# Performance work log

Measured on AMD Instinct MI355X. Metric: run time of the kernel, lower is better.

The kernel has to match this reference:

```python
import jax, jax.numpy as jnp
import numpy as np

B, N, F_IN, F_OUT = 8, 2048, 256, 64
ALPHA = 0.2          # LeakyReLU negative slope
NEG_INF = -9e15      # matches -9000000000000000.0 in the torch code


def setup_inputs() -> dict:
    key = jax.random.key(0)
    k = jax.random.split(key, 7)
    x = jax.random.normal(k[0], (B, N, F_IN), dtype=jnp.float32)
    adj = jax.random.randint(k[1], (B, N, N), 0, 2, dtype=jnp.int32)
    # W: nn.Linear(in_features, out_features)
    W = jax.random.normal(k[2], (F_IN, F_OUT), dtype=jnp.float32) / np.sqrt(F_IN)
    b_W = jax.random.normal(k[3], (F_OUT,), dtype=jnp.float32) * 0.01
    # a: nn.Linear(2*out_features, 1); decomposed as a_src (first F_OUT rows,
    # multiplies h_i) and a_dst (last F_OUT rows, multiplies h_j) + bias.
    a_src = jax.random.normal(k[4], (F_OUT,), dtype=jnp.float32) / np.sqrt(2 * F_OUT)
    a_dst = jax.random.normal(k[5], (F_OUT,), dtype=jnp.float32) / np.sqrt(2 * F_OUT)
    a_b = jax.random.normal(k[6], (), dtype=jnp.float32) * 0.01
    return {"x": x, "adj": adj, "W": W, "b_W": b_W,
            "a_src": a_src, "a_dst": a_dst, "a_b": a_b}


def reference(x, adj, W, b_W, a_src, a_dst, a_b):
    # h = W(input): [B, N, F_OUT]
    h = jnp.einsum('bnf,fo->bno', x, W) + b_W
    # Additive attention decomposition: a([h_i || h_j]) = a_src.h_i + a_dst.h_j + b
    # (avoids materializing the [B, N, N, 2F] concat tensor of the original)
    src = jnp.einsum('bno,o->bn', h, a_src)  # row term  (h_i)
    dst = jnp.einsum('bno,o->bn', h, a_dst)  # col term  (h_j)
    e = jax.nn.leaky_relu(src[:, :, None] + dst[:, None, :] + a_b, ALPHA)  # [B,N,N]
    e = jnp.where(adj > 0, e, NEG_INF)
    attention = jax.nn.softmax(e, axis=2)
    h_prime = jnp.einsum('bij,bjo->bio', attention, h)  # [B, N, F_OUT]
    return jax.nn.elu(h_prime)  # concat=True branch
```

## Files before the change

kernel.cpp:

```cpp
#include <hip/hip_runtime.h>

#define B_   8
#define N_   2048
#define FIN  256
#define FOUT 64
#define ALPHA 0.2f

typedef __attribute__((ext_vector_type(8))) short bf16x8;
typedef __attribute__((ext_vector_type(8))) unsigned short u16x8;
typedef __attribute__((ext_vector_type(4))) unsigned short u16x4;
typedef __attribute__((ext_vector_type(4))) float f32x4;

__device__ __forceinline__ float b2f(unsigned short u) {
    union { unsigned int u; float f; } v; v.u = ((unsigned int)u) << 16; return v.f;
}
__device__ __forceinline__ unsigned short f2b(float f) {
    union { float f; unsigned int u; } v; v.f = f;
    unsigned int r = v.u + 0x7FFFu + ((v.u >> 16) & 1u);
    return (unsigned short)(r >> 16);
}

__global__ __launch_bounds__(256) void k_hgemm_tr(
    const float* __restrict__ x, const float* __restrict__ W,
    const float* __restrict__ bW, const float* __restrict__ asrc,
    const float* __restrict__ adst,
    unsigned short* __restrict__ hT, float* __restrict__ src, float* __restrict__ dst)
{
    __shared__ unsigned short tileT[FOUT * 20];
    __shared__ float as_s[FOUT], ad_s[FOUT];

    const int tid = threadIdx.x;
    const int wv = tid >> 6, lane = tid & 63;
    const int quad = lane >> 4, col = lane & 15;
    const int f = wv * 16 + col;

    if (tid < FOUT) { as_s[tid] = asrc[tid]; ad_s[tid] = adst[tid]; }

    bf16x8 Bf[8];
    #pragma unroll
    for (int kk = 0; kk < 8; ++kk) {
        bf16x8 t;
        #pragma unroll
        for (int j = 0; j < 8; ++j)
            t[j] = (short)f2b(W[(kk * 32 + quad * 8 + j) * FOUT + f]);
        Bf[kk] = t;
    }
    const float bias = bW[f];
    const int r0 = blockIdx.x * 16;
    const int b = r0 >> 11;
    const int j0b = r0 & (N_ - 1);

    f32x4 acc = {0.f, 0.f, 0.f, 0.f};
    #pragma unroll
    for (int kk = 0; kk < 8; ++kk) {
        const float* xp = x + (size_t)(r0 + col) * FIN + kk * 32 + quad * 8;
        float4 x0 = *(const float4*)xp;
        float4 x1 = *(const float4*)(xp + 4);
        bf16x8 Af;
        Af[0] = (short)f2b(x0.x); Af[1] = (short)f2b(x0.y);
        Af[2] = (short)f2b(x0.z); Af[3] = (short)f2b(x0.w);
        Af[4] = (short)f2b(x1.x); Af[5] = (short)f2b(x1.y);
        Af[6] = (short)f2b(x1.z); Af[7] = (short)f2b(x1.w);
        acc = __builtin_amdgcn_mfma_f32_16x16x32_bf16(Af, Bf[kk], acc, 0, 0, 0);
    }
    #pragma unroll
    for (int reg = 0; reg < 4; ++reg)
        tileT[f * 20 + quad * 4 + reg] = f2b(acc[reg] + bias);
    __syncthreads();

    {
        const int i = tid >> 4, fb = (tid & 15) * 4;
        float sp = 0.f, dp = 0.f;
        #pragma unroll
        for (int k = 0; k < 4; ++k) {
            float hv = b2f(tileT[(fb + k) * 20 + i]);
            sp += hv * as_s[fb + k]; dp += hv * ad_s[fb + k];
        }
        sp += __shfl_xor(sp, 1); sp += __shfl_xor(sp, 2);
        sp += __shfl_xor(sp, 4); sp += __shfl_xor(sp, 8);
        dp += __shfl_xor(dp, 1); dp += __shfl_xor(dp, 2);
        dp += __shfl_xor(dp, 4); dp += __shfl_xor(dp, 8);
        if ((tid & 15) == 0) { src[r0 + i] = sp; dst[r0 + i] = dp; }
    }
    {
        const int fq = tid >> 2, ic = (tid & 3) * 4;
        unsigned short* op = hT + (size_t)(b * FOUT + fq) * N_ + j0b + ic;
        *(u16x4*)op = *(const u16x4*)&tileT[fq * 20 + ic];
    }
}

#define ATT_TILE(Aa,Ab,Ac,Ad, Da,Db,Dc,Dd, BfC, BfN, BUF, JT)                          \
{                                                                                      \
    const int av[16] = {Aa.x,Aa.y,Aa.z,Aa.w, Ab.x,Ab.y,Ab.z,Ab.w,                      \
                        Ac.x,Ac.y,Ac.z,Ac.w, Ad.x,Ad.y,Ad.z,Ad.w};                     \
    const float dv[16] = {Da.x,Da.y,Da.z,Da.w, Db.x,Db.y,Db.z,Db.w,                    \
                          Dc.x,Dc.y,Dc.z,Dc.w, Dd.x,Dd.y,Dd.z,Dd.w};                   \
    u16x8 p0, p1; float ls = 0.f;                                                      \
    _Pragma("unroll")                                                                  \
    for (int k = 0; k < 16; ++k) {                                                     \
        float e = srci + dv[k];                                                        \
        e = e > 0.f ? e : ALPHA * e;                                                   \
        float wval = av[k] > 0 ? __expf(e) : 0.f;                                      \
        unsigned short wb = f2b(wval);                                                 \
        ls += b2f(wb);         \
        if (k < 8) p0[k] = wb; else p1[k - 8] = wb;                                    \
    }                                                                                  \
    lsum += ls;                                                                        \
    {   unsigned short* q = &w_s[BUF][il * 136 + jg * 16];                             \
        *(u16x8*)q = p0; *(u16x8*)(q + 8) = p1; }                                      \
    {                  \
        const int jn = (((JT) + 2) & 15) * 128;                                        \
        Aa = *(const int4*)(adjbase + jn);                                             \
        Ab = *(const int4*)(adjbase + jn + 4);                                         \
        Ac = *(const int4*)(adjbase + jn + 8);                                         \
        Ad = *(const int4*)(adjbase + jn + 12);                                        \
        Da = *(const float4*)(dstbase + jn);                                           \
        Db = *(const float4*)(dstbase + jn + 4);                                       \
        Dc = *(const float4*)(dstbase + jn + 8);                                       \
        Dd = *(const float4*)(dstbase + jn + 12); }                                    \
                  \
    asm volatile("s_waitcnt lgkmcnt(0)\n\ts_barrier" ::: "memory");                    \
    {                        \
        const int jn = (((JT) + 1) & 15) * 128;                                        \
        BfN[0] = *(const bf16x8*)(hfbase + jn);                                        \
        BfN[1] = *(const bf16x8*)(hfbase + jn + 32);                                   \
        BfN[2] = *(const bf16x8*)(hfbase + jn + 64);                                   \
        BfN[3] = *(const bf16x8*)(hfbase + jn + 96); }                                 \
    _Pragma("unroll")                                                                  \
    for (int kk = 0; kk < 4; ++kk) {                                                   \
        bf16x8 A0 = *(const bf16x8*)&w_s[BUF][col * 136 + kk * 32 + quad * 8];         \
        bf16x8 A1 = *(const bf16x8*)&w_s[BUF][(16 + col) * 136 + kk * 32 + quad * 8];  \
        acc0 = __builtin_amdgcn_mfma_f32_16x16x32_bf16(A0, BfC[kk], acc0, 0, 0, 0);    \
        acc1 = __builtin_amdgcn_mfma_f32_16x16x32_bf16(A1, BfC[kk], acc1, 0, 0, 0);    \
    }                                                                                  \
}

__global__ __launch_bounds__(256) void k_attn(
    const int* __restrict__ adj, const float* __restrict__ src, const float* __restrict__ dst,
    const unsigned short* __restrict__ hT, const float* __restrict__ abp,
    float* __restrict__ out)
{
    __shared__ unsigned short w_s[2][32 * 136];
    __shared__ float src_s[32];
    __shared__ float l_s[32];

    const int tid = threadIdx.x;
    const int wv = tid >> 6, lane = tid & 63;
    const int quad = lane >> 4, col = lane & 15;
    const int b = blockIdx.x >> 6;
    const int i0 = (blockIdx.x & 63) * 32;

    if (tid < 32) src_s[tid] = src[b * N_ + i0 + tid];
    __syncthreads();

    const int il = tid >> 3, jg = tid & 7;
    const float srci = src_s[il] + abp[0];
    const int* adjbase = adj + (size_t)(b * N_ + i0 + il) * N_ + jg * 16;
    const float* dstbase = dst + b * N_ + jg * 16;
    const unsigned short* hfbase = hT + (size_t)(b * FOUT + wv * 16 + col) * N_ + quad * 8;

    int4 a0 = *(const int4*)(adjbase);
    int4 a1 = *(const int4*)(adjbase + 4);
    int4 a2 = *(const int4*)(adjbase + 8);
    int4 a3 = *(const int4*)(adjbase + 12);
    int4 a4 = *(const int4*)(adjbase + 128);
    int4 a5 = *(const int4*)(adjbase + 132);
    int4 a6 = *(const int4*)(adjbase + 136);
    int4 a7 = *(const int4*)(adjbase + 140);
    float4 d0 = *(const float4*)(dstbase);
    float4 d1 = *(const float4*)(dstbase + 4);
    float4 d2 = *(const float4*)(dstbase + 8);
    float4 d3 = *(const float4*)(dstbase + 12);
    float4 d4 = *(const float4*)(dstbase + 128);
    float4 d5 = *(const float4*)(dstbase + 132);
    float4 d6 = *(const float4*)(dstbase + 136);
    float4 d7 = *(const float4*)(dstbase + 140);
    bf16x8 bfE[4], bfO[4];
    bfE[0] = *(const bf16x8*)(hfbase);
    bfE[1] = *(const bf16x8*)(hfbase + 32);
    bfE[2] = *(const bf16x8*)(hfbase + 64);
    bfE[3] = *(const bf16x8*)(hfbase + 96);

    float lsum = 0.f;
    f32x4 acc0 = {0, 0, 0, 0}, acc1 = {0, 0, 0, 0};

    for (int it = 0; it < 8; ++it) {
        const int jt = it * 2;
        ATT_TILE(a0, a1, a2, a3, d0, d1, d2, d3, bfE, bfO, 0, jt)
        ATT_TILE(a4, a5, a6, a7, d4, d5, d6, d7, bfO, bfE, 1, jt + 1)
    }

    lsum += __shfl_xor(lsum, 1);
    lsum += __shfl_xor(lsum, 2);
    lsum += __shfl_xor(lsum, 4);
    if (jg == 0) l_s[il] = lsum;
    __syncthreads();

    #pragma unroll
    for (int m = 0; m < 2; ++m) {
        f32x4 a = m ? acc1 : acc0;
        #pragma unroll
        for (int reg = 0; reg < 4; ++reg) {
            int row = m * 16 + quad * 4 + reg;
            float l = l_s[row];
            l = l > 0.f ? l : 1.f;
            float v = a[reg] / l;
            v = v > 0.f ? v : (__expf(v) - 1.f);
            out[(size_t)(b * N_ + i0 + row) * FOUT + wv * 16 + col] = v;
        }
    }
}

extern "C" void kernel_launch(void* const* d_in, const int* in_sizes, int n_in,
                              void* d_out, int out_size, void* d_ws, size_t ws_size,
                              hipStream_t stream)
{
    const float* x    = (const float*)d_in[0];
    const int*   adj  = (const int*)d_in[1];
    const float* W    = (const float*)d_in[2];
    const float* bW   = (const float*)d_in[3];
    const float* asrc = (const float*)d_in[4];
    const float* adst = (const float*)d_in[5];
    const float* abp  = (const float*)d_in[6];
    float* out = (float*)d_out;

    char* ws = (char*)d_ws;
    unsigned short* hT = (unsigned short*)ws;
    float* src = (float*)(ws + (size_t)2 * 1024 * 1024);
    float* dst = (float*)(ws + (size_t)2 * 1024 * 1024 + 64 * 1024);

    k_hgemm_tr<<<1024, 256, 0, stream>>>(x, W, bW, asrc, adst, hT, src, dst);
    k_attn<<<512, 256, 0, stream>>>(adj, src, dst, hT, abp, out);
}
```

Before: 223.1 us.

## Pack adjacency into bitmask in projection kernel and read bits in attention

The first kernel now also streams the int32 adjacency matrix and compacts it into a 1-bit-per-entry mask in workspace, using wave shuffles to assemble 32-bit words. The attention kernel then loads one 16-bit mask per tile instead of four int4 vectors, which cuts its global traffic and register pressure. Total adjacency bytes read stay the same, now moved into the first kernel, plus an extra 4 MB mask write and read. The intent is to make the attention loop lighter and overlap the adjacency streaming with the projection GEMM.

```diff
diff --git a/kernel.cpp b/kernel.cpp
--- a/kernel.cpp
+++ b/kernel.cpp
@@ -21,10 +21,11 @@
 }
 
 __global__ __launch_bounds__(256) void k_hgemm_tr(
-    const float* __restrict__ x, const float* __restrict__ W,
-    const float* __restrict__ bW, const float* __restrict__ asrc,
-    const float* __restrict__ adst,
-    unsigned short* __restrict__ hT, float* __restrict__ src, float* __restrict__ dst)
+    const float* __restrict__ x, const int* __restrict__ adj,
+    const float* __restrict__ W, const float* __restrict__ bW,
+    const float* __restrict__ asrc, const float* __restrict__ adst,
+    unsigned short* __restrict__ hT, float* __restrict__ src, float* __restrict__ dst,
+    unsigned int* __restrict__ adjm)
 {
     __shared__ unsigned short tileT[FOUT * 20];
     __shared__ float as_s[FOUT], ad_s[FOUT];
@@ -87,20 +88,44 @@
         unsigned short* op = hT + (size_t)(b * FOUT + fq) * N_ + j0b + ic;
         *(u16x4*)op = *(const u16x4*)&tileT[fq * 20 + ic];
     }
-}
-
-#define ATT_TILE(Aa,Ab,Ac,Ad, Da,Db,Dc,Dd, BfC, BfN, BUF, JT)                          \
+
+    {
+        const int ln = lane;
+        const size_t wave_words0 = (size_t)blockIdx.x * 1024 + wv * 16;
+        #pragma unroll 4
+        for (int r = 0; r < 16; ++r) {
+            const size_t wb0 = wave_words0 + (size_t)r * 64;
+            const int* ap = adj + wb0 * 32 + ln * 8;
+            int4 v0 = *(const int4*)ap;
+            int4 v1 = *(const int4*)(ap + 4);
+            unsigned int bits = 0;
+            bits |= (unsigned int)(v0.x > 0) << 0;
+            bits |= (unsigned int)(v0.y > 0) << 1;
+            bits |= (unsigned int)(v0.z > 0) << 2;
+            bits |= (unsigned int)(v0.w > 0) << 3;
+            bits |= (unsigned int)(v1.x > 0) << 4;
+            bits |= (unsigned int)(v1.y > 0) << 5;
+            bits |= (unsigned int)(v1.z > 0) << 6;
+            bits |= (unsigned int)(v1.w > 0) << 7;
+            unsigned int s1 = __shfl_xor(bits, 1);
+            unsigned int w1 = (bits << ((ln & 1) * 8)) | (s1 << ((~ln & 1) * 8));
+            unsigned int s2 = __shfl_xor(w1, 2);
+            unsigned int w2 = (w1 << ((ln & 2) * 8)) | (s2 << ((~ln & 2) * 8));
+            if ((ln & 3) == 0) adjm[wb0 + (ln >> 2)] = w2;
+        }
+    }
+}
+
+#define ATT_TILE(MC, Dc0,Dc1,Dc2,Dc3, MN, Dn0,Dn1,Dn2,Dn3, BfC, BfN, BUF, JT)         \
 {                                                                                      \
-    const int av[16] = {Aa.x,Aa.y,Aa.z,Aa.w, Ab.x,Ab.y,Ab.z,Ab.w,                      \
-                        Ac.x,Ac.y,Ac.z,Ac.w, Ad.x,Ad.y,Ad.z,Ad.w};                     \
-    const float dv[16] = {Da.x,Da.y,Da.z,Da.w, Db.x,Db.y,Db.z,Db.w,                    \
-                          Dc.x,Dc.y,Dc.z,Dc.w, Dd.x,Dd.y,Dd.z,Dd.w};                   \
+    const float dv[16] = {Dc0.x,Dc0.y,Dc0.z,Dc0.w, Dc1.x,Dc1.y,Dc1.z,Dc1.w,            \
+                          Dc2.x,Dc2.y,Dc2.z,Dc2.w, Dc3.x,Dc3.y,Dc3.z,Dc3.w};           \
     u16x8 p0, p1; float ls = 0.f;                                                      \
     _Pragma("unroll")                                                                  \
     for (int k = 0; k < 16; ++k) {                                                     \
         float e = srci + dv[k];                                                        \
         e = e > 0.f ? e : ALPHA * e;                                                   \
-        float wval = av[k] > 0 ? __expf(e) : 0.f;                                      \
+        float wval = ((MC >> k) & 1u) ? __expf(e) : 0.f;                               \
         unsigned short wb = f2b(wval);                                                 \
         ls += b2f(wb);         \
         if (k < 8) p0[k] = wb; else p1[k - 8] = wb;                                    \
@@ -108,17 +133,14 @@
     lsum += ls;                                                                        \
     {   unsigned short* q = &w_s[BUF][il * 136 + jg * 16];                             \
         *(u16x8*)q = p0; *(u16x8*)(q + 8) = p1; }                                      \
-    {                  \
-        const int jn = (((JT) + 2) & 15) * 128;                                        \
-        Aa = *(const int4*)(adjbase + jn);                                             \
-        Ab = *(const int4*)(adjbase + jn + 4);                                         \
-        Ac = *(const int4*)(adjbase + jn + 8);                                         \
-        Ad = *(const int4*)(adjbase + jn + 12);                                        \
-        Da = *(const float4*)(dstbase + jn);                                           \
-        Db = *(const float4*)(dstbase + jn + 4);                                       \
-        Dc = *(const float4*)(dstbase + jn + 8);                                       \
-        Dd = *(const float4*)(dstbase + jn + 12); }                                    \
-                  \
+    {                       \
+        const int jn = ((JT) + 1) & 15;                                                \
+        MN = mbase[jn * 8];                                                            \
+        Dn0 = *(const float4*)(dstbase + jn * 128);                                    \
+        Dn1 = *(const float4*)(dstbase + jn * 128 + 4);                                \
+        Dn2 = *(const float4*)(dstbase + jn * 128 + 8);                                \
+        Dn3 = *(const float4*)(dstbase + jn * 128 + 12); }                             \
+                 \
     asm volatile("s_waitcnt lgkmcnt(0)\n\ts_barrier" ::: "memory");                    \
     {                        \
         const int jn = (((JT) + 1) & 15) * 128;                                        \
@@ -136,9 +158,9 @@
 }
 
 __global__ __launch_bounds__(256) void k_attn(
-    const int* __restrict__ adj, const float* __restrict__ src, const float* __restrict__ dst,
-    const unsigned short* __restrict__ hT, const float* __restrict__ abp,
-    float* __restrict__ out)
+    const unsigned short* __restrict__ adjm, const float* __restrict__ src,
+    const float* __restrict__ dst, const unsigned short* __restrict__ hT,
+    const float* __restrict__ abp, float* __restrict__ out)
 {
     __shared__ unsigned short w_s[2][32 * 136];
     __shared__ float src_s[32];
@@ -155,26 +177,16 @@
 
     const int il = tid >> 3, jg = tid & 7;
     const float srci = src_s[il] + abp[0];
-    const int* adjbase = adj + (size_t)(b * N_ + i0 + il) * N_ + jg * 16;
+    const unsigned short* mbase = adjm + (size_t)(b * N_ + i0 + il) * 128 + jg;
     const float* dstbase = dst + b * N_ + jg * 16;
     const unsigned short* hfbase = hT + (size_t)(b * FOUT + wv * 16 + col) * N_ + quad * 8;
 
-    int4 a0 = *(const int4*)(adjbase);
-    int4 a1 = *(const int4*)(adjbase + 4);
-    int4 a2 = *(const int4*)(adjbase + 8);
-    int4 a3 = *(const int4*)(adjbase + 12);
-    int4 a4 = *(const int4*)(adjbase + 128);
-    int4 a5 = *(const int4*)(adjbase + 132);
-    int4 a6 = *(const int4*)(adjbase + 136);
-    int4 a7 = *(const int4*)(adjbase + 140);
-    float4 d0 = *(const float4*)(dstbase);
-    float4 d1 = *(const float4*)(dstbase + 4);
-    float4 d2 = *(const float4*)(dstbase + 8);
-    float4 d3 = *(const float4*)(dstbase + 12);
-    float4 d4 = *(const float4*)(dstbase + 128);
-    float4 d5 = *(const float4*)(dstbase + 132);
-    float4 d6 = *(const float4*)(dstbase + 136);
-    float4 d7 = *(const float4*)(dstbase + 140);
+    unsigned int mE = mbase[0], mO;
+    float4 dE0 = *(const float4*)(dstbase);
+    float4 dE1 = *(const float4*)(dstbase + 4);
+    float4 dE2 = *(const float4*)(dstbase + 8);
+    float4 dE3 = *(const float4*)(dstbase + 12);
+    float4 dO0, dO1, dO2, dO3;
     bf16x8 bfE[4], bfO[4];
     bfE[0] = *(const bf16x8*)(hfbase);
     bfE[1] = *(const bf16x8*)(hfbase + 32);
@@ -186,8 +198,8 @@
 
     for (int it = 0; it < 8; ++it) {
         const int jt = it * 2;
-        ATT_TILE(a0, a1, a2, a3, d0, d1, d2, d3, bfE, bfO, 0, jt)
-        ATT_TILE(a4, a5, a6, a7, d4, d5, d6, d7, bfO, bfE, 1, jt + 1)
+        ATT_TILE(mE, dE0, dE1, dE2, dE3, mO, dO0, dO1, dO2, dO3, bfE, bfO, 0, jt)
+        ATT_TILE(mO, dO0, dO1, dO2, dO3, mE, dE0, dE1, dE2, dE3, bfO, bfE, 1, jt + 1)
     }
 
     lsum += __shfl_xor(lsum, 1);
@@ -228,7 +240,8 @@
     unsigned short* hT = (unsigned short*)ws;
     float* src = (float*)(ws + (size_t)2 * 1024 * 1024);
     float* dst = (float*)(ws + (size_t)2 * 1024 * 1024 + 64 * 1024);
-
-    k_hgemm_tr<<<1024, 256, 0, stream>>>(x, W, bW, asrc, adst, hT, src, dst);
-    k_attn<<<512, 256, 0, stream>>>(adj, src, dst, hT, abp, out);
-}
+    unsigned int* adjm = (unsigned int*)(ws + (size_t)4 * 1024 * 1024);
+
+    k_hgemm_tr<<<1024, 256, 0, stream>>>(x, adj, W, bW, asrc, adst, hT, src, dst, adjm);
+    k_attn<<<512, 256, 0, stream>>>((const unsigned short*)adjm, src, dst, hT, abp, out);
+}
```

Result: slower. 244.9 us (+9.8%).

## Split attention over column chunks with partial sums and a reduce kernel

Applied to the files above, without the earlier changes.

The attention kernel now splits each row block's 2048 columns into four 512-column slices, launching four times as many blocks. Each block writes unnormalized partial outputs and row-sum partials to workspace, and a new reduce kernel sums them, normalizes, and applies ELU. The aim is to raise occupancy and memory-level parallelism on the adjacency stream, which the 512-block grid left underused. The cost is extra workspace traffic for the partials, an additional launch, and dst values loaded per tile instead of prefetched.

```diff
diff --git a/kernel.cpp b/kernel.cpp
--- a/kernel.cpp
+++ b/kernel.cpp
@@ -89,12 +89,17 @@
     }
 }
 
-#define ATT_TILE(Aa,Ab,Ac,Ad, Da,Db,Dc,Dd, BfC, BfN, BUF, JT)                          \
+#define ATT_TILE(Aa,Ab,Ac,Ad, An0,An1,An2,An3, BfC, BfN, BUF, JT)                      \
 {                                                                                      \
+                   \
+    const float4 Dv0 = *(const float4*)(dstbase + (JT) * 128);                         \
+    const float4 Dv1 = *(const float4*)(dstbase + (JT) * 128 + 4);                     \
+    const float4 Dv2 = *(const float4*)(dstbase + (JT) * 128 + 8);                     \
+    const float4 Dv3 = *(const float4*)(dstbase + (JT) * 128 + 12);                    \
     const int av[16] = {Aa.x,Aa.y,Aa.z,Aa.w, Ab.x,Ab.y,Ab.z,Ab.w,                      \
                         Ac.x,Ac.y,Ac.z,Ac.w, Ad.x,Ad.y,Ad.z,Ad.w};                     \
-    const float dv[16] = {Da.x,Da.y,Da.z,Da.w, Db.x,Db.y,Db.z,Db.w,                    \
-                          Dc.x,Dc.y,Dc.z,Dc.w, Dd.x,Dd.y,Dd.z,Dd.w};                   \
+    const float dv[16] = {Dv0.x,Dv0.y,Dv0.z,Dv0.w, Dv1.x,Dv1.y,Dv1.z,Dv1.w,            \
+                          Dv2.x,Dv2.y,Dv2.z,Dv2.w, Dv3.x,Dv3.y,Dv3.z,Dv3.w};           \
     u16x8 p0, p1; float ls = 0.f;                                                      \
     _Pragma("unroll")                                                                  \
     for (int k = 0; k < 16; ++k) {                                                     \
@@ -108,20 +113,16 @@
     lsum += ls;                                                                        \
     {   unsigned short* q = &w_s[BUF][il * 136 + jg * 16];                             \
         *(u16x8*)q = p0; *(u16x8*)(q + 8) = p1; }                                      \
-    {                  \
-        const int jn = (((JT) + 2) & 15) * 128;                                        \
-        Aa = *(const int4*)(adjbase + jn);                                             \
-        Ab = *(const int4*)(adjbase + jn + 4);                                         \
-        Ac = *(const int4*)(adjbase + jn + 8);                                         \
-        Ad = *(const int4*)(adjbase + jn + 12);                                        \
-        Da = *(const float4*)(dstbase + jn);                                           \
-        Db = *(const float4*)(dstbase + jn + 4);                                       \
-        Dc = *(const float4*)(dstbase + jn + 8);                                       \
-        Dd = *(const float4*)(dstbase + jn + 12); }                                    \
-                  \
+    {                          \
+        const int jn = (((JT) + 1) & 3) * 128;                                         \
+        An0 = *(const int4*)(adjbase + jn);                                            \
+        An1 = *(const int4*)(adjbase + jn + 4);                                        \
+        An2 = *(const int4*)(adjbase + jn + 8);                                        \
+        An3 = *(const int4*)(adjbase + jn + 12); }                                     \
+                                   \
     asm volatile("s_waitcnt lgkmcnt(0)\n\ts_barrier" ::: "memory");                    \
-    {                        \
-        const int jn = (((JT) + 1) & 15) * 128;                                        \
+    {                                        \
+        const int jn = (((JT) + 1) & 3) * 128;                                         \
         BfN[0] = *(const bf16x8*)(hfbase + jn);                                        \
         BfN[1] = *(const bf16x8*)(hfbase + jn + 32);                                   \
         BfN[2] = *(const bf16x8*)(hfbase + jn + 64);                                   \
@@ -135,46 +136,38 @@
     }                                                                                  \
 }
 
-__global__ __launch_bounds__(256) void k_attn(
-    const int* __restrict__ adj, const float* __restrict__ src, const float* __restrict__ dst,
-    const unsigned short* __restrict__ hT, const float* __restrict__ abp,
-    float* __restrict__ out)
+__global__ __launch_bounds__(256, 4) void k_attn(
+    const int* __restrict__ adj, const float* __restrict__ src,
+    const float* __restrict__ dst, const unsigned short* __restrict__ hT,
+    const float* __restrict__ abp,
+    float* __restrict__ pnum, float* __restrict__ pden)
 {
     __shared__ unsigned short w_s[2][32 * 136];
     __shared__ float src_s[32];
-    __shared__ float l_s[32];
 
     const int tid = threadIdx.x;
     const int wv = tid >> 6, lane = tid & 63;
     const int quad = lane >> 4, col = lane & 15;
-    const int b = blockIdx.x >> 6;
-    const int i0 = (blockIdx.x & 63) * 32;
+    const int s4 = blockIdx.x & 3;
+    const int g  = blockIdx.x >> 2;
+    const int b  = g >> 6;
+    const int i0 = (g & 63) * 32;
+    const int j0 = s4 * 512;
 
     if (tid < 32) src_s[tid] = src[b * N_ + i0 + tid];
     __syncthreads();
 
     const int il = tid >> 3, jg = tid & 7;
     const float srci = src_s[il] + abp[0];
-    const int* adjbase = adj + (size_t)(b * N_ + i0 + il) * N_ + jg * 16;
-    const float* dstbase = dst + b * N_ + jg * 16;
-    const unsigned short* hfbase = hT + (size_t)(b * FOUT + wv * 16 + col) * N_ + quad * 8;
-
-    int4 a0 = *(const int4*)(adjbase);
-    int4 a1 = *(const int4*)(adjbase + 4);
-    int4 a2 = *(const int4*)(adjbase + 8);
-    int4 a3 = *(const int4*)(adjbase + 12);
-    int4 a4 = *(const int4*)(adjbase + 128);
-    int4 a5 = *(const int4*)(adjbase + 132);
-    int4 a6 = *(const int4*)(adjbase + 136);
-    int4 a7 = *(const int4*)(adjbase + 140);
-    float4 d0 = *(const float4*)(dstbase);
-    float4 d1 = *(const float4*)(dstbase + 4);
-    float4 d2 = *(const float4*)(dstbase + 8);
-    float4 d3 = *(const float4*)(dstbase + 12);
-    float4 d4 = *(const float4*)(dstbase + 128);
-    float4 d5 = *(const float4*)(dstbase + 132);
-    float4 d6 = *(const float4*)(dstbase + 136);
-    float4 d7 = *(const float4*)(dstbase + 140);
+    const int* adjbase = adj + (size_t)(b * N_ + i0 + il) * N_ + j0 + jg * 16;
+    const float* dstbase = dst + b * N_ + j0 + jg * 16;
+    const unsigned short* hfbase = hT + (size_t)(b * FOUT + wv * 16 + col) * N_ + j0 + quad * 8;
+
+    int4 aE0 = *(const int4*)(adjbase);
+    int4 aE1 = *(const int4*)(adjbase + 4);
+    int4 aE2 = *(const int4*)(adjbase + 8);
+    int4 aE3 = *(const int4*)(adjbase + 12);
+    int4 aO0, aO1, aO2, aO3;
     bf16x8 bfE[4], bfO[4];
     bfE[0] = *(const bf16x8*)(hfbase);
     bfE[1] = *(const bf16x8*)(hfbase + 32);
@@ -184,30 +177,47 @@
     float lsum = 0.f;
     f32x4 acc0 = {0, 0, 0, 0}, acc1 = {0, 0, 0, 0};
 
-    for (int it = 0; it < 8; ++it) {
-        const int jt = it * 2;
-        ATT_TILE(a0, a1, a2, a3, d0, d1, d2, d3, bfE, bfO, 0, jt)
-        ATT_TILE(a4, a5, a6, a7, d4, d5, d6, d7, bfO, bfE, 1, jt + 1)
-    }
+    ATT_TILE(aE0, aE1, aE2, aE3, aO0, aO1, aO2, aO3, bfE, bfO, 0, 0)
+    ATT_TILE(aO0, aO1, aO2, aO3, aE0, aE1, aE2, aE3, bfO, bfE, 1, 1)
+    ATT_TILE(aE0, aE1, aE2, aE3, aO0, aO1, aO2, aO3, bfE, bfO, 0, 2)
+    ATT_TILE(aO0, aO1, aO2, aO3, aE0, aE1, aE2, aE3, bfO, bfE, 1, 3)
 
     lsum += __shfl_xor(lsum, 1);
     lsum += __shfl_xor(lsum, 2);
     lsum += __shfl_xor(lsum, 4);
-    if (jg == 0) l_s[il] = lsum;
-    __syncthreads();
-
+    if (jg == 0) pden[(size_t)blockIdx.x * 32 + il] = lsum;
+
+    float* pb = pnum + (size_t)blockIdx.x * 2048 + wv * 16 + col;
     #pragma unroll
     for (int m = 0; m < 2; ++m) {
         f32x4 a = m ? acc1 : acc0;
         #pragma unroll
-        for (int reg = 0; reg < 4; ++reg) {
-            int row = m * 16 + quad * 4 + reg;
-            float l = l_s[row];
-            l = l > 0.f ? l : 1.f;
-            float v = a[reg] / l;
-            v = v > 0.f ? v : (__expf(v) - 1.f);
-            out[(size_t)(b * N_ + i0 + row) * FOUT + wv * 16 + col] = v;
+        for (int reg = 0; reg < 4; ++reg)
+            pb[(m * 16 + quad * 4 + reg) * 64] = a[reg];
+    }
+}
+
+__global__ __launch_bounds__(256) void k_reduce(
+    const float* __restrict__ pnum, const float* __restrict__ pden,
+    float* __restrict__ out)
+{
+    const int g = blockIdx.x;
+    const int tid = threadIdx.x;
+    const int f = tid & 63, ro = tid >> 6;
+    const size_t base = (size_t)g * 4 * 2048;
+    #pragma unroll
+    for (int rr = 0; rr < 8; ++rr) {
+        const int row = ro * 8 + rr;
+        float num = 0.f, den = 0.f;
+        #pragma unroll
+        for (int s = 0; s < 4; ++s) {
+            num += pnum[base + (size_t)s * 2048 + row * 64 + f];
+            den += pden[(size_t)(g * 4 + s) * 32 + row];
         }
+        den = den > 0.f ? den : 1.f;
+        float v = num / den;
+        v = v > 0.f ? v : (__expf(v) - 1.f);
+        out[((size_t)g * 32 + row) * 64 + f] = v;
     }
 }
 
@@ -226,9 +236,12 @@
 
     char* ws = (char*)d_ws;
     unsigned short* hT = (unsigned short*)ws;
-    float* src = (float*)(ws + (size_t)2 * 1024 * 1024);
-    float* dst = (float*)(ws + (size_t)2 * 1024 * 1024 + 64 * 1024);
+    float* src  = (float*)(ws + (size_t)2 * 1024 * 1024);
+    float* dst  = (float*)(ws + (size_t)2 * 1024 * 1024 + 64 * 1024);
+    float* pnum = (float*)(ws + (size_t)4 * 1024 * 1024);
+    float* pden = (float*)(ws + (size_t)21 * 1024 * 1024);
 
     k_hgemm_tr<<<1024, 256, 0, stream>>>(x, W, bW, asrc, adst, hT, src, dst);
-    k_attn<<<512, 256, 0, stream>>>(adj, src, dst, hT, abp, out);
-}
+    k_attn<<<2048, 256, 0, stream>>>(adj, src, dst, hT, abp, pnum, pden);
+    k_reduce<<<512, 256, 0, stream>>>(pnum, pden, out);
+}
```

After: 243.9 us. +9.3%, slower.
